# Optimization experiments

Hardware: AMD Instinct MI355X
Metric: run time of the kernel (lower is better)

Reference implementation:

```python
import jax, jax.numpy as jnp
import numpy as np

N = 50000   # nodes
E = 800000  # edges
G = 64      # graphs in batch
H = 64      # hidden_dim
IN = 4      # input_dim (degree-derived features)


def setup_inputs() -> dict:
    key = jax.random.key(0)
    ks = jax.random.split(key, 9)
    src = jax.random.randint(ks[0], (E,), 0, N, dtype=jnp.int32)
    dst = jax.random.randint(ks[1], (E,), 0, N, dtype=jnp.int32)
    graph_ids = jnp.sort(jax.random.randint(ks[2], (N,), 0, G, dtype=jnp.int32))

    def glorot(k, shape):
        fan_in = shape[0]
        return jax.random.normal(k, shape, jnp.float32) / np.float32(np.sqrt(fan_in))

    return dict(
        src=src, dst=dst, graph_ids=graph_ids,
        W1=glorot(ks[3], (IN, H)), b1=jnp.zeros((H,), jnp.float32),
        W2=glorot(ks[4], (H, H)),  b2=jnp.zeros((H,), jnp.float32),
        W3=glorot(ks[5], (H, H)),  b3=jnp.zeros((H,), jnp.float32),
        W4=glorot(ks[6], (H, H)),  b4=jnp.zeros((H,), jnp.float32),
        Wout=glorot(ks[7], (H, 1)), bout=jnp.zeros((1,), jnp.float32),
    )


def _graph_conv(h, src, dst, norm_src, norm_dst, W, b):
    # DGL GraphConv, norm='both': D_dst^{-1/2} * A^T * (D_src^{-1/2} * h) @ W + b
    m = (h * norm_src)[src]                              # [E, F] gather
    agg = jax.ops.segment_sum(m, dst, num_segments=N)    # [N, F] scatter-add
    return (agg * norm_dst) @ W + b


def reference(src, dst, graph_ids, W1, b1, W2, b2, W3, b3, W4, b4, Wout, bout):
    ones_e = jnp.ones((E,), jnp.float32)
    in_deg = jax.ops.segment_sum(ones_e, dst, num_segments=N)   # [N]
    out_deg = jax.ops.segment_sum(ones_e, src, num_segments=N)  # [N]

    # degree-derived node features (exactly as in forward)
    h1 = in_deg[:, None]
    h2 = (in_deg - 3.0 > 0).astype(jnp.float32)[:, None]
    h3 = 3.0 / h1
    h4 = (in_deg - 4.0 > 0).astype(jnp.float32)[:, None]
    h_ = jnp.concatenate([h1, h2, h3, h4], axis=1)               # [N, 4]

    # symmetric norms (DGL clamps degree to >= 1)
    norm_src = jnp.clip(out_deg, 1.0, None)[:, None] ** -0.5     # [N, 1]
    norm_dst = jnp.clip(in_deg, 1.0, None)[:, None] ** -0.5      # [N, 1]

    h = jax.nn.relu(_graph_conv(h_, src, dst, norm_src, norm_dst, W1, b1))
    h = jax.nn.relu(_graph_conv(h, src, dst, norm_src, norm_dst, W2, b2))
    h = jax.nn.relu(_graph_conv(h, src, dst, norm_src, norm_dst, W3, b3))
    h = jax.nn.relu(_graph_conv(h, src, dst, norm_src, norm_dst, W4, b4))

    # dgl.mean_nodes: per-graph mean pooling
    node_counts = jax.ops.segment_sum(jnp.ones((N,), jnp.float32), graph_ids, num_segments=G)
    graph_emb = jax.ops.segment_sum(h, graph_ids, num_segments=G) / node_counts[:, None]

    # dropout = identity at inference
    return jax.nn.sigmoid(graph_emb @ Wout + bout)               # [G, 1]
```

## Files before the change

### kernel.cpp

```cpp
#include <hip/hip_runtime.h>
#include <hip/hip_fp8.h>
#include <math.h>

#define N_NODES 50000
#define N_EDGES 800000
#define NP 4
#define NS 64
#define PSZ (N_NODES / NP)
#define SSZ (N_EDGES / NS)
#define NB 196

typedef _Float16 half8 __attribute__((ext_vector_type(8)));
typedef float floatx4 __attribute__((ext_vector_type(4)));

__device__ __forceinline__ unsigned char f_to_fp8(float f) {
    __hip_fp8_e4m3 q(f);
    return (unsigned char)q.__x;
}
__device__ __forceinline__ float fp8_to_f(unsigned char u) {
    __hip_fp8_e4m3 q;
    q.__x = (__hip_fp8_storage_t)u;
    return (float)q;
}

__global__ __launch_bounds__(256) void hist_wt_kernel(const int* __restrict__ src,
                                                      const int* __restrict__ dst,
                                                      unsigned char* __restrict__ inpart,
                                                      unsigned char* __restrict__ outpart,
                                                      unsigned char* __restrict__ rank,
                                                      const float* __restrict__ W2,
                                                      const float* __restrict__ W3,
                                                      const float* __restrict__ W4,
                                                      _Float16* __restrict__ WT,
                                                      float* __restrict__ gacc) {
    __shared__ int h[PSZ + 4];
    if (blockIdx.x >= NP * NS) {
        int wb = blockIdx.x - NP * NS;
        if (wb < 48) {
            int i = wb * 256 + threadIdx.x;
            if (i < 3 * 4096) {
                int l = i >> 12;
                int r = i & 4095;
                int k = r >> 6, n = r & 63;
                const float* W = (l == 0) ? W2 : (l == 1) ? W3 : W4;
                WT[l * 4096 + n * 64 + k] = (_Float16)W[r];
            }
        } else {
            for (int i = threadIdx.x; i < 64 * 64 + 64; i += 256) gacc[i] = 0.0f;
        }
        return;
    }
    int p = blockIdx.x / NS, s = blockIdx.x % NS;
    for (int i = threadIdx.x; i < (PSZ + 4) / 4; i += 256)
        ((int4*)h)[i] = make_int4(0, 0, 0, 0);
    __syncthreads();
    int lo = p * PSZ;
    int ebase = s * SSZ;
    const int4* d4 = (const int4*)(dst + ebase);
    const int4* s4 = (const int4*)(src + ebase);
    unsigned char* rk = rank + ebase;
    for (int i = threadIdx.x; i < SSZ / 4; i += 256) {
        int4 d = d4[i];
        int4 sv = s4[i];
        int t;
        t = d.x - lo;  if ((unsigned)t < PSZ) rk[4 * i + 0] = (unsigned char)(atomicAdd(&h[t], 1) & 0xffff);
        t = d.y - lo;  if ((unsigned)t < PSZ) rk[4 * i + 1] = (unsigned char)(atomicAdd(&h[t], 1) & 0xffff);
        t = d.z - lo;  if ((unsigned)t < PSZ) rk[4 * i + 2] = (unsigned char)(atomicAdd(&h[t], 1) & 0xffff);
        t = d.w - lo;  if ((unsigned)t < PSZ) rk[4 * i + 3] = (unsigned char)(atomicAdd(&h[t], 1) & 0xffff);
        t = sv.x - lo; if ((unsigned)t < PSZ) atomicAdd(&h[t], 0x10000);
        t = sv.y - lo; if ((unsigned)t < PSZ) atomicAdd(&h[t], 0x10000);
        t = sv.z - lo; if ((unsigned)t < PSZ) atomicAdd(&h[t], 0x10000);
        t = sv.w - lo; if ((unsigned)t < PSZ) atomicAdd(&h[t], 0x10000);
    }
    __syncthreads();
    unsigned char* ip = inpart + (size_t)s * N_NODES + lo;
    unsigned char* op = outpart + (size_t)s * N_NODES + lo;
    for (int i = threadIdx.x; i < PSZ / 2; i += 256) {
        int v0 = h[2 * i], v1 = h[2 * i + 1];
        uchar2 iv, ov;
        iv.x = (unsigned char)(v0 & 0xff);
        iv.y = (unsigned char)(v1 & 0xff);
        ov.x = (unsigned char)((v0 >> 16) & 0xff);
        ov.y = (unsigned char)((v1 >> 16) & 0xff);
        ((uchar2*)ip)[i] = iv;
        ((uchar2*)op)[i] = ov;
    }
}

__global__ void scan_block_feat_kernel(unsigned char* __restrict__ inpart,
                                       const unsigned char* __restrict__ outpart,
                                       const int* __restrict__ graph_ids,
                                       int* __restrict__ row_start, int* __restrict__ blk_sums,
                                       float* __restrict__ norm_src, float* __restrict__ norm_dst,
                                       uchar4* __restrict__ hs0, float* __restrict__ gcnt, int N) {
    __shared__ int ghist[64];
    if (threadIdx.x < 64) ghist[threadIdx.x] = 0;
    int i = blockIdx.x * 256 + threadIdx.x;
    int din_i = 0, dout_i = 0;
    if (i < N) {
        unsigned char run = 0;
#pragma unroll
        for (int s = 0; s < NS; ++s) {
            unsigned char c = inpart[(size_t)s * N_NODES + i];
            inpart[(size_t)s * N_NODES + i] = run;
            run = (unsigned char)(run + c);
            dout_i += outpart[(size_t)s * N_NODES + i];
        }
        din_i = (int)run;
        float din = (float)din_i;
        float dout = (float)dout_i;
        float ns = 1.0f / sqrtf(fmaxf(dout, 1.0f));
        float nd = 1.0f / sqrtf(fmaxf(din, 1.0f));
        norm_src[i] = ns;
        norm_dst[i] = nd;
        float h1 = din;
        float h2 = (din - 3.0f > 0.0f) ? 1.0f : 0.0f;
        float h3 = 3.0f / din;
        float h4 = (din - 4.0f > 0.0f) ? 1.0f : 0.0f;
        uchar4 q;
        q.x = f_to_fp8(h1 * ns);
        q.y = f_to_fp8(h2 * ns);
        q.z = f_to_fp8(h3 * ns);
        q.w = f_to_fp8(h4 * ns);
        hs0[i] = q;
    }
    __syncthreads();
    if (i < N) atomicAdd(&ghist[graph_ids[i]], 1);
    int lane = threadIdx.x & 63;
    int wid = threadIdx.x >> 6;
    int x = din_i;
#pragma unroll
    for (int off = 1; off < 64; off <<= 1) {
        int t = __shfl_up(x, off);
        if (lane >= off) x += t;
    }
    __shared__ int wsum[4];
    if (lane == 63) wsum[wid] = x;
    __syncthreads();
    int woff = 0;
    for (int w = 0; w < wid; ++w) woff += wsum[w];
    int incl = x + woff;
    if (i < N) row_start[i] = incl - din_i;
    if (threadIdx.x == 255) blk_sums[blockIdx.x] = incl;
    if (threadIdx.x < 64 && ghist[threadIdx.x] > 0)
        atomicAdd(&gcnt[threadIdx.x], (float)ghist[threadIdx.x]);
}

__global__ void row_add_kernel(int* __restrict__ row_start,
                               const int* __restrict__ blk_sums, int N) {
    __shared__ int sOff[256];
    int t = threadIdx.x;
    int v = (t < NB) ? blk_sums[t] : 0;
    int lane = t & 63;
    int wid = t >> 6;
    int x = v;
#pragma unroll
    for (int off = 1; off < 64; off <<= 1) {
        int tt = __shfl_up(x, off);
        if (lane >= off) x += tt;
    }
    __shared__ int wsum[4];
    if (lane == 63) wsum[wid] = x;
    __syncthreads();
    int woff = 0;
    for (int w = 0; w < wid; ++w) woff += wsum[w];
    sOff[t] = x + woff - v;
    __syncthreads();
    int i = blockIdx.x * 256 + threadIdx.x;
    if (blockIdx.x == 0 && threadIdx.x == 0) row_start[N] = N_EDGES;
    if (i < N) row_start[i] += sOff[blockIdx.x];
}

__global__ __launch_bounds__(256) void csr_fill_kernel(const int* __restrict__ src,
                                                       const int* __restrict__ dst,
                                                       const int* __restrict__ row_start,
                                                       const unsigned char* __restrict__ inpart,
                                                       const unsigned char* __restrict__ rank,
                                                       unsigned short* __restrict__ csr_src) {
    int i = blockIdx.x * 256 + threadIdx.x;
    if (i >= N_EDGES / 4) return;
    int4 d = ((const int4*)dst)[i];
    int4 sv = ((const int4*)src)[i];
    uchar4 rk = ((const uchar4*)rank)[i];
    int s = (4 * i) / SSZ;
    const unsigned char* pref = inpart + (size_t)s * N_NODES;
    csr_src[row_start[d.x] + (int)pref[d.x] + (int)rk.x] = (unsigned short)sv.x;
    csr_src[row_start[d.y] + (int)pref[d.y] + (int)rk.y] = (unsigned short)sv.y;
    csr_src[row_start[d.z] + (int)pref[d.z] + (int)rk.z] = (unsigned short)sv.z;
    csr_src[row_start[d.w] + (int)pref[d.w] + (int)rk.w] = (unsigned short)sv.w;
}

__global__ void conv4_kernel(const uchar4* __restrict__ hs0,
                             const int* __restrict__ row_start,
                             const unsigned short* __restrict__ csr_src,
                             const float* __restrict__ norm_src,
                             const float* __restrict__ norm_dst,
                             const float* __restrict__ W, const float* __restrict__ b,
                             unsigned char* __restrict__ out, int N) {
    __shared__ float sW[4 * 64];
    __shared__ float sb[64];
    sW[threadIdx.x] = W[threadIdx.x];
    if (threadIdx.x < 64) sb[threadIdx.x] = b[threadIdx.x];
    __syncthreads();
    int lane = threadIdx.x & 63;
    int wid = threadIdx.x >> 6;
    int v = blockIdx.x * 4 + wid;
    if (v >= N) return;
    int rs = row_start[v], re = row_start[v + 1];
    float ax = 0.f, ay = 0.f, az = 0.f, aw = 0.f;
    for (int e = rs + lane; e < re; e += 64) {
        uchar4 f = hs0[csr_src[e]];
        ax += fp8_to_f(f.x); ay += fp8_to_f(f.y);
        az += fp8_to_f(f.z); aw += fp8_to_f(f.w);
    }
#pragma unroll
    for (int off = 32; off; off >>= 1) {
        ax += __shfl_xor(ax, off);
        ay += __shfl_xor(ay, off);
        az += __shfl_xor(az, off);
        aw += __shfl_xor(aw, off);
    }
    float nd = norm_dst[v];
    float r = sb[lane] + nd * (ax * sW[lane] + ay * sW[64 + lane] +
                               az * sW[128 + lane] + aw * sW[192 + lane]);
    r = fmaxf(r, 0.0f) * norm_src[v];
    out[(size_t)v * 64 + lane] = f_to_fp8(r);
}

#define LOADIDX(MY, E0)  MY = (int)csr_src[(E0) + (lane & 15)];

#define GATHER(T, MY)                                                   \
    _Pragma("unroll")                                                   \
    for (int j = 0; j < 16; ++j) {                                      \
        unsigned uu = (unsigned)__builtin_amdgcn_readlane(MY, j);       \
        if (uu >= (unsigned)N_NODES) uu = 0;                            \
        T[j] = hs_in[(uu << 6) + (unsigned)lane];                       \
    }

#define ACCUM(T)                                                        \
    _Pragma("unroll")                                                   \
    for (int j = 0; j < 16; ++j) {                                      \
        while (ecur == bound) {                                         \
            float ndc = __uint_as_float(                                \
                (unsigned)__builtin_amdgcn_readlane((int)nd8u, cur - vbase)); \
            sAgg[wavei][cur - vbase][lane] = (_Float16)(acc * ndc);     \
            acc = 0.0f;                                                 \
            ++cur;                                                      \
            bound = (cur < vend)                                        \
                        ? __builtin_amdgcn_readlane(rb8, cur - vbase)   \
                        : 0x7fffffff;                                   \
        }                                                               \
        acc += fp8_to_f(T[j]);                                         \
        ++ecur;                                                         \
    }

__global__ __launch_bounds__(256) void conv64_kernel(
        const unsigned char* __restrict__ hs_in,
        const int* __restrict__ row_start,
        const unsigned short* __restrict__ csr_src,
        const float* __restrict__ norm_src,
        const float* __restrict__ norm_dst,
        const _Float16* __restrict__ WT, const float* __restrict__ b,
        unsigned char* __restrict__ out8,
        const int* __restrict__ graph_ids, float* __restrict__ gacc,
        int do_pool, int N) {
    __shared__ _Float16 sAgg[4][16][72];
    const int lane = threadIdx.x & 63;
    const int wavei = __builtin_amdgcn_readfirstlane(threadIdx.x >> 6);
    const int vbase = blockIdx.x * 32 + wavei * 8;
    if (vbase >= N) return;

    const int vend = vbase + 8;
    const int rb8 = row_start[vbase + 1 + (lane & 7)];
    const unsigned nd8u = __float_as_uint(norm_dst[vbase + (lane & 7)]);
    const unsigned ns8u = __float_as_uint(norm_src[vbase + (lane & 7)]);
    const int rs = row_start[vbase];
    const int re = __builtin_amdgcn_readlane(rb8, 7);
    int cur = vbase;
    int bound = __builtin_amdgcn_readlane(rb8, 0);
    int ecur = rs;
    float acc = 0.0f;
    int nbp = (re - rs + 15) >> 4;
    int e = rs;
    int myA, myB;
    unsigned char tA[16], tB[16];

    if (nbp > 0) {
        LOADIDX(myA, e);
        GATHER(tA, myA);
        LOADIDX(myB, e + 16);
        int k = 0;
        while (k + 2 <= nbp) {
            GATHER(tB, myB);
            LOADIDX(myA, e + 32);
            ACCUM(tA);
            if (k + 2 < nbp) {
                GATHER(tA, myA);
                LOADIDX(myB, e + 48);
            }
            ACCUM(tB);
            k += 2; e += 32;
        }
        if (k < nbp) { ACCUM(tA); }
    }
    while (cur < vend) {
        float ndc = __uint_as_float(
            (unsigned)__builtin_amdgcn_readlane((int)nd8u, cur - vbase));
        sAgg[wavei][cur - vbase][lane] = (_Float16)(acc * ndc);
        acc = 0.0f;
        ++cur;
    }

    const int l15 = lane & 15;
    const int quad = lane >> 4;
    const _Float16* aRow = &sAgg[wavei][l15][quad * 8];
    half8 a0 = *(const half8*)(aRow);
    half8 a1 = *(const half8*)(aRow + 32);

    floatx4 c[4];
#pragma unroll
    for (int nt = 0; nt < 4; ++nt) c[nt] = (floatx4){0.f, 0.f, 0.f, 0.f};

#pragma unroll
    for (int nt = 0; nt < 4; ++nt) {
        const _Float16* bp = WT + ((size_t)(nt * 16 + l15)) * 64 + quad * 8;
        half8 b0 = *(const half8*)bp;
        half8 b1 = *(const half8*)(bp + 32);
        c[nt] = __builtin_amdgcn_mfma_f32_16x16x32_f16(a0, b0, c[nt], 0, 0, 0);
        c[nt] = __builtin_amdgcn_mfma_f32_16x16x32_f16(a1, b1, c[nt], 0, 0, 0);
    }

    if (do_pool) {
        int g0 = graph_ids[vbase];
        int g7 = graph_ids[vbase + 7];
        if (g0 == g7) {
#pragma unroll
            for (int nt = 0; nt < 4; ++nt) {
                float bias = b[nt * 16 + l15];
                float fsum = 0.0f;
                if (quad < 2) {
#pragma unroll
                    for (int r = 0; r < 4; ++r)
                        fsum += fmaxf(c[nt][r] + bias, 0.0f);
                }
                fsum += __shfl_xor(fsum, 16);
                if (quad == 0)
                    atomicAdd(&gacc[g0 * 64 + nt * 16 + l15], fsum);
            }
        } else {
#pragma unroll
            for (int nt = 0; nt < 4; ++nt) {
                float bias = b[nt * 16 + l15];
#pragma unroll
                for (int r = 0; r < 4; ++r) {
                    int m = quad * 4 + r;
                    if (m < 8) {
                        int v = vbase + m;
                        float val = fmaxf(c[nt][r] + bias, 0.0f);
                        atomicAdd(&gacc[graph_ids[v] * 64 + nt * 16 + l15], val);
                    }
                }
            }
        }
    } else {
#pragma unroll
        for (int nt = 0; nt < 4; ++nt) {
            float bias = b[nt * 16 + l15];
#pragma unroll
            for (int r = 0; r < 4; ++r) {
                int m = quad * 4 + r;
                int v = vbase + m;
                if (m < 8 && v < N) {
                    float nsv = __uint_as_float(
                        (unsigned)__builtin_amdgcn_readlane((int)ns8u, m));
                    float val = fmaxf(c[nt][r] + bias, 0.0f) * nsv;
                    out8[(size_t)v * 64 + nt * 16 + l15] = f_to_fp8(val);
                }
            }
        }
    }
}

__global__ void pool2_kernel(const float* __restrict__ gacc, const float* __restrict__ gcnt,
                             const float* __restrict__ Wout, const float* __restrict__ bout,
                             float* __restrict__ out) {
    int lane = threadIdx.x & 63;
    int g = blockIdx.x * 4 + (threadIdx.x >> 6);
    float p = (gacc[g * 64 + lane] / gcnt[g]) * Wout[lane];
#pragma unroll
    for (int off = 32; off; off >>= 1) p += __shfl_xor(p, off);
    if (lane == 0) out[g] = 1.0f / (1.0f + expf(-(p + bout[0])));
}

extern "C" void kernel_launch(void* const* d_in, const int* in_sizes, int n_in,
                              void* d_out, int out_size, void* d_ws, size_t ws_size,
                              hipStream_t stream) {
    const int* src = (const int*)d_in[0];
    const int* dst = (const int*)d_in[1];
    const int* graph_ids = (const int*)d_in[2];
    const float* W1 = (const float*)d_in[3];
    const float* b1 = (const float*)d_in[4];
    const float* W2 = (const float*)d_in[5];
    const float* b2 = (const float*)d_in[6];
    const float* W3 = (const float*)d_in[7];
    const float* b3 = (const float*)d_in[8];
    const float* W4 = (const float*)d_in[9];
    const float* b4 = (const float*)d_in[10];
    const float* Wout = (const float*)d_in[11];
    const float* bout = (const float*)d_in[12];
    float* out = (float*)d_out;

    const int N = N_NODES, E = N_EDGES;

    unsigned char* buf8A = (unsigned char*)d_ws;
    unsigned char* buf8B = buf8A + (size_t)N * 64;
    _Float16* WT   = (_Float16*)(buf8B + (size_t)N * 64);
    float* gacc = (float*)(WT + 3 * 4096);
    float* gcnt = gacc + 64 * 64;
    unsigned char* hs0 = (unsigned char*)(gcnt + 64);
    float* norm_src = (float*)(hs0 + (size_t)N * 4);
    float* norm_dst = norm_src + N;
    unsigned short* csr_src = (unsigned short*)(norm_dst + N);
    int* row_start = (int*)(csr_src + E);
    int* blk_sums  = row_start + (N + 1);
    unsigned char* inpart  = (unsigned char*)(blk_sums + NB + 1);
    unsigned char* outpart = inpart + (size_t)NS * N;
    unsigned char* rank    = outpart + (size_t)NS * N;

    hist_wt_kernel<<<NP * NS + 49, 256, 0, stream>>>(src, dst, inpart, outpart, rank,
                                                     W2, W3, W4, WT, gacc);
    scan_block_feat_kernel<<<NB, 256, 0, stream>>>(inpart, outpart, graph_ids,
                                                   row_start, blk_sums,
                                                   norm_src, norm_dst, (uchar4*)hs0, gcnt, N);
    row_add_kernel<<<NB, 256, 0, stream>>>(row_start, blk_sums, N);
    csr_fill_kernel<<<(E / 4 + 255) / 256, 256, 0, stream>>>(src, dst, row_start, inpart,
                                                             rank, csr_src);

    conv4_kernel<<<(N + 3) / 4, 256, 0, stream>>>((const uchar4*)hs0, row_start, csr_src,
                                                  norm_src, norm_dst, W1, b1, buf8A, N);
    const int CB = (N + 31) / 32;
    conv64_kernel<<<CB, 256, 0, stream>>>(buf8A, row_start, csr_src, norm_src, norm_dst,
                                          WT + 0 * 4096, b2, buf8B, graph_ids, gacc, 0, N);
    conv64_kernel<<<CB, 256, 0, stream>>>(buf8B, row_start, csr_src, norm_src, norm_dst,
                                          WT + 1 * 4096, b3, buf8A, graph_ids, gacc, 0, N);
    conv64_kernel<<<CB, 256, 0, stream>>>(buf8A, row_start, csr_src, norm_src, norm_dst,
                                          WT + 2 * 4096, b4, (unsigned char*)nullptr,
                                          graph_ids, gacc, 1, N);

    pool2_kernel<<<16, 256, 0, stream>>>(gacc, gcnt, Wout, bout, out);
}
```

Baseline: 211.6 us.

## Use single-wave blocks and triple-buffered gathers in conv64 kernel

Conv64 now launches one 64-thread wave per block covering 8 nodes instead of four waves per block, which shrinks shared memory to one wave's tile and lets the scheduler place waves independently. The edge-gather loop moves from double to triple buffering, so two gather batches are in flight while a third is accumulated, hiding more gather latency. The cost is more registers per thread for the extra buffer, which can lower occupancy, and many more small blocks to launch. The remainder handling after the loop is reworked to drain up to two pending buffers.

```diff
diff --git a/kernel.cpp b/kernel.cpp
--- a/kernel.cpp
+++ b/kernel.cpp
@@ -243,7 +243,7 @@
         while (ecur == bound) {                                         \
             float ndc = __uint_as_float(                                \
                 (unsigned)__builtin_amdgcn_readlane((int)nd8u, cur - vbase)); \
-            sAgg[wavei][cur - vbase][lane] = (_Float16)(acc * ndc);     \
+            sAgg[cur - vbase][lane] = (_Float16)(acc * ndc);            \
             acc = 0.0f;                                                 \
             ++cur;                                                      \
             bound = (cur < vend)                                        \
@@ -254,7 +254,7 @@
         ++ecur;                                                         \
     }
 
-__global__ __launch_bounds__(256) void conv64_kernel(
+__global__ __launch_bounds__(64) void conv64_kernel(
         const unsigned char* __restrict__ hs_in,
         const int* __restrict__ row_start,
         const unsigned short* __restrict__ csr_src,
@@ -264,10 +264,9 @@
         unsigned char* __restrict__ out8,
         const int* __restrict__ graph_ids, float* __restrict__ gacc,
         int do_pool, int N) {
-    __shared__ _Float16 sAgg[4][16][72];
+    __shared__ _Float16 sAgg[16][72];
     const int lane = threadIdx.x & 63;
-    const int wavei = __builtin_amdgcn_readfirstlane(threadIdx.x >> 6);
-    const int vbase = blockIdx.x * 32 + wavei * 8;
+    const int vbase = blockIdx.x * 8;
     if (vbase >= N) return;
 
     const int vend = vbase + 8;
@@ -282,38 +281,37 @@
     float acc = 0.0f;
     int nbp = (re - rs + 15) >> 4;
     int e = rs;
-    int myA, myB;
-    unsigned char tA[16], tB[16];
+    int my0, my1, my2;
+    unsigned char t0[16], t1[16], t2[16];
 
     if (nbp > 0) {
-        LOADIDX(myA, e);
-        GATHER(tA, myA);
-        LOADIDX(myB, e + 16);
+        LOADIDX(my0, e);
+        GATHER(t0, my0);
+        LOADIDX(my1, e + 16);
+        GATHER(t1, my1);
+        LOADIDX(my2, e + 32);
         int k = 0;
-        while (k + 2 <= nbp) {
-            GATHER(tB, myB);
-            LOADIDX(myA, e + 32);
-            ACCUM(tA);
-            if (k + 2 < nbp) {
-                GATHER(tA, myA);
-                LOADIDX(myB, e + 48);
-            }
-            ACCUM(tB);
-            k += 2; e += 32;
+        while (k + 3 <= nbp) {
+            GATHER(t2, my2);  LOADIDX(my0, e + 48);  ACCUM(t0);
+            GATHER(t0, my0);  LOADIDX(my1, e + 64);  ACCUM(t1);
+            GATHER(t1, my1);  LOADIDX(my2, e + 80);  ACCUM(t2);
+            k += 3; e += 48;
         }
-        if (k < nbp) { ACCUM(tA); }
+        int r = nbp - k;
+        if (r >= 1) { ACCUM(t0); }
+        if (r >= 2) { ACCUM(t1); }
     }
     while (cur < vend) {
         float ndc = __uint_as_float(
             (unsigned)__builtin_amdgcn_readlane((int)nd8u, cur - vbase));
-        sAgg[wavei][cur - vbase][lane] = (_Float16)(acc * ndc);
+        sAgg[cur - vbase][lane] = (_Float16)(acc * ndc);
         acc = 0.0f;
         ++cur;
     }
 
     const int l15 = lane & 15;
     const int quad = lane >> 4;
-    const _Float16* aRow = &sAgg[wavei][l15][quad * 8];
+    const _Float16* aRow = &sAgg[l15][quad * 8];
     half8 a0 = *(const half8*)(aRow);
     half8 a1 = *(const half8*)(aRow + 32);
 
@@ -438,14 +436,14 @@
 
     conv4_kernel<<<(N + 3) / 4, 256, 0, stream>>>((const uchar4*)hs0, row_start, csr_src,
                                                   norm_src, norm_dst, W1, b1, buf8A, N);
-    const int CB = (N + 31) / 32;
-    conv64_kernel<<<CB, 256, 0, stream>>>(buf8A, row_start, csr_src, norm_src, norm_dst,
-                                          WT + 0 * 4096, b2, buf8B, graph_ids, gacc, 0, N);
-    conv64_kernel<<<CB, 256, 0, stream>>>(buf8B, row_start, csr_src, norm_src, norm_dst,
-                                          WT + 1 * 4096, b3, buf8A, graph_ids, gacc, 0, N);
-    conv64_kernel<<<CB, 256, 0, stream>>>(buf8A, row_start, csr_src, norm_src, norm_dst,
-                                          WT + 2 * 4096, b4, (unsigned char*)nullptr,
-                                          graph_ids, gacc, 1, N);
+    const int CB = N / 8;
+    conv64_kernel<<<CB, 64, 0, stream>>>(buf8A, row_start, csr_src, norm_src, norm_dst,
+                                         WT + 0 * 4096, b2, buf8B, graph_ids, gacc, 0, N);
+    conv64_kernel<<<CB, 64, 0, stream>>>(buf8B, row_start, csr_src, norm_src, norm_dst,
+                                         WT + 1 * 4096, b3, buf8A, graph_ids, gacc, 0, N);
+    conv64_kernel<<<CB, 64, 0, stream>>>(buf8A, row_start, csr_src, norm_src, norm_dst,
+                                         WT + 2 * 4096, b4, (unsigned char*)nullptr,
+                                         graph_ids, gacc, 1, N);
 
     pool2_kernel<<<16, 256, 0, stream>>>(gacc, gcnt, Wout, bout, out);
 }
```

New measurement: 230.3 us. 1.09x slower.

## Restructure conv64 gather to one node per 16-lane group with 4-byte loads

Applied to the files above, without the earlier changes.

Each wave now handles four nodes, one per 16-lane group, and each lane loads four fp8 features as a 32-bit word. This replaces the serial per-wave walk over 8 nodes, which used per-byte gathers and segment-boundary branching. Blocks now cover 16 nodes that share one block-wide aggregation tile; each wave computes one 16-column slice of the output with two MFMAs after a __syncthreads. Load imbalance between groups in a wave, since lanes run to the maximum degree, and the extra barrier are the tradeoffs.

```diff
diff --git a/kernel.cpp b/kernel.cpp
--- a/kernel.cpp
+++ b/kernel.cpp
@@ -227,33 +227,6 @@
     out[(size_t)v * 64 + lane] = f_to_fp8(r);
 }
 
-#define LOADIDX(MY, E0)  MY = (int)csr_src[(E0) + (lane & 15)];
-
-#define GATHER(T, MY)                                                   \
-    _Pragma("unroll")                                                   \
-    for (int j = 0; j < 16; ++j) {                                      \
-        unsigned uu = (unsigned)__builtin_amdgcn_readlane(MY, j);       \
-        if (uu >= (unsigned)N_NODES) uu = 0;                            \
-        T[j] = hs_in[(uu << 6) + (unsigned)lane];                       \
-    }
-
-#define ACCUM(T)                                                        \
-    _Pragma("unroll")                                                   \
-    for (int j = 0; j < 16; ++j) {                                      \
-        while (ecur == bound) {                                         \
-            float ndc = __uint_as_float(                                \
-                (unsigned)__builtin_amdgcn_readlane((int)nd8u, cur - vbase)); \
-            sAgg[wavei][cur - vbase][lane] = (_Float16)(acc * ndc);     \
-            acc = 0.0f;                                                 \
-            ++cur;                                                      \
-            bound = (cur < vend)                                        \
-                        ? __builtin_amdgcn_readlane(rb8, cur - vbase)   \
-                        : 0x7fffffff;                                   \
-        }                                                               \
-        acc += fp8_to_f(T[j]);                                         \
-        ++ecur;                                                         \
-    }
-
 __global__ __launch_bounds__(256) void conv64_kernel(
         const unsigned char* __restrict__ hs_in,
         const int* __restrict__ row_start,
@@ -264,119 +237,118 @@
         unsigned char* __restrict__ out8,
         const int* __restrict__ graph_ids, float* __restrict__ gacc,
         int do_pool, int N) {
-    __shared__ _Float16 sAgg[4][16][72];
+    __shared__ _Float16 sAgg[16][72];
     const int lane = threadIdx.x & 63;
     const int wavei = __builtin_amdgcn_readfirstlane(threadIdx.x >> 6);
-    const int vbase = blockIdx.x * 32 + wavei * 8;
-    if (vbase >= N) return;
-
-    const int vend = vbase + 8;
-    const int rb8 = row_start[vbase + 1 + (lane & 7)];
-    const unsigned nd8u = __float_as_uint(norm_dst[vbase + (lane & 7)]);
-    const unsigned ns8u = __float_as_uint(norm_src[vbase + (lane & 7)]);
-    const int rs = row_start[vbase];
-    const int re = __builtin_amdgcn_readlane(rb8, 7);
-    int cur = vbase;
-    int bound = __builtin_amdgcn_readlane(rb8, 0);
-    int ecur = rs;
-    float acc = 0.0f;
-    int nbp = (re - rs + 15) >> 4;
-    int e = rs;
-    int myA, myB;
-    unsigned char tA[16], tB[16];
-
-    if (nbp > 0) {
-        LOADIDX(myA, e);
-        GATHER(tA, myA);
-        LOADIDX(myB, e + 16);
-        int k = 0;
-        while (k + 2 <= nbp) {
-            GATHER(tB, myB);
-            LOADIDX(myA, e + 32);
-            ACCUM(tA);
-            if (k + 2 < nbp) {
-                GATHER(tA, myA);
-                LOADIDX(myB, e + 48);
-            }
-            ACCUM(tB);
-            k += 2; e += 32;
-        }
-        if (k < nbp) { ACCUM(tA); }
-    }
-    while (cur < vend) {
-        float ndc = __uint_as_float(
-            (unsigned)__builtin_amdgcn_readlane((int)nd8u, cur - vbase));
-        sAgg[wavei][cur - vbase][lane] = (_Float16)(acc * ndc);
-        acc = 0.0f;
-        ++cur;
-    }
+    const int l16 = lane & 15;
+    const int gsel = (lane >> 4);
+    const int vblock = blockIdx.x * 16;
+    const int node = vblock + wavei * 4 + gsel;
+
+    const int rs = row_start[node];
+    const int deg = row_start[node + 1] - rs;
+
+    int ncg = (deg + 15) >> 4;
+    int m1 = max(ncg, __shfl_xor(ncg, 16));
+    int ncw = max(m1, __shfl_xor(m1, 32));
+
+    float acc0 = 0.f, acc1 = 0.f, acc2 = 0.f, acc3 = 0.f;
+    const int blane = (lane & 48);
+
+    int pos = rs + l16;
+    unsigned pc = (unsigned)pos;
+    if (pc > (unsigned)(N_EDGES - 1)) pc = N_EDGES - 1;
+    int idx = (int)csr_src[pc];
+
+    for (int c = 0; c < ncw; ++c) {
+        int posN = rs + (c + 1) * 16 + l16;
+        unsigned pn = (unsigned)posN;
+        if (pn > (unsigned)(N_EDGES - 1)) pn = N_EDGES - 1;
+        int idxN = (int)csr_src[pn];
+
+        unsigned tv0, tv1, tv2, tv3, tv4, tv5, tv6, tv7;
+        unsigned tv8, tv9, tv10, tv11, tv12, tv13, tv14, tv15;
+#define GLOAD(J, TV)                                                        \
+        {                                                                   \
+            int si = __shfl(idx, blane + (J));                              \
+            TV = *(const unsigned*)(hs_in + (((size_t)(unsigned)si) << 6)   \
+                                    + (l16 << 2));                          \
+        }
+        GLOAD(0, tv0)   GLOAD(1, tv1)   GLOAD(2, tv2)   GLOAD(3, tv3)
+        GLOAD(4, tv4)   GLOAD(5, tv5)   GLOAD(6, tv6)   GLOAD(7, tv7)
+        GLOAD(8, tv8)   GLOAD(9, tv9)   GLOAD(10, tv10) GLOAD(11, tv11)
+        GLOAD(12, tv12) GLOAD(13, tv13) GLOAD(14, tv14) GLOAD(15, tv15)
+#undef GLOAD
+        int cbase = c * 16;
+#define ACC(J, TV)                                                          \
+        {                                                                   \
+            float mk = (cbase + (J) < deg) ? 1.0f : 0.0f;                   \
+            acc0 += mk * fp8_to_f((unsigned char)(TV & 0xff));              \
+            acc1 += mk * fp8_to_f((unsigned char)((TV >> 8) & 0xff));       \
+            acc2 += mk * fp8_to_f((unsigned char)((TV >> 16) & 0xff));      \
+            acc3 += mk * fp8_to_f((unsigned char)((TV >> 24) & 0xff));      \
+        }
+        ACC(0, tv0)   ACC(1, tv1)   ACC(2, tv2)   ACC(3, tv3)
+        ACC(4, tv4)   ACC(5, tv5)   ACC(6, tv6)   ACC(7, tv7)
+        ACC(8, tv8)   ACC(9, tv9)   ACC(10, tv10) ACC(11, tv11)
+        ACC(12, tv12) ACC(13, tv13) ACC(14, tv14) ACC(15, tv15)
+#undef ACC
+        idx = idxN;
+    }
+
+    float nd = norm_dst[node];
+    _Float16 f0 = (_Float16)(acc0 * nd);
+    _Float16 f1 = (_Float16)(acc1 * nd);
+    _Float16 f2 = (_Float16)(acc2 * nd);
+    _Float16 f3 = (_Float16)(acc3 * nd);
+    _Float16* rowp = &sAgg[wavei * 4 + gsel][l16 * 4];
+    rowp[0] = f0; rowp[1] = f1; rowp[2] = f2; rowp[3] = f3;
+    __syncthreads();
 
     const int l15 = lane & 15;
     const int quad = lane >> 4;
-    const _Float16* aRow = &sAgg[wavei][l15][quad * 8];
+    const _Float16* aRow = &sAgg[l15][quad * 8];
     half8 a0 = *(const half8*)(aRow);
     half8 a1 = *(const half8*)(aRow + 32);
 
-    floatx4 c[4];
-#pragma unroll
-    for (int nt = 0; nt < 4; ++nt) c[nt] = (floatx4){0.f, 0.f, 0.f, 0.f};
-
-#pragma unroll
-    for (int nt = 0; nt < 4; ++nt) {
-        const _Float16* bp = WT + ((size_t)(nt * 16 + l15)) * 64 + quad * 8;
-        half8 b0 = *(const half8*)bp;
-        half8 b1 = *(const half8*)(bp + 32);
-        c[nt] = __builtin_amdgcn_mfma_f32_16x16x32_f16(a0, b0, c[nt], 0, 0, 0);
-        c[nt] = __builtin_amdgcn_mfma_f32_16x16x32_f16(a1, b1, c[nt], 0, 0, 0);
-    }
+    const _Float16* bp = WT + ((size_t)(wavei * 16 + l15)) * 64 + quad * 8;
+    half8 b0 = *(const half8*)bp;
+    half8 b1 = *(const half8*)(bp + 32);
+
+    floatx4 cc = (floatx4){0.f, 0.f, 0.f, 0.f};
+    cc = __builtin_amdgcn_mfma_f32_16x16x32_f16(a0, b0, cc, 0, 0, 0);
+    cc = __builtin_amdgcn_mfma_f32_16x16x32_f16(a1, b1, cc, 0, 0, 0);
+
+    const int col = wavei * 16 + l15;
+    float bias = b[col];
 
     if (do_pool) {
-        int g0 = graph_ids[vbase];
-        int g7 = graph_ids[vbase + 7];
-        if (g0 == g7) {
-#pragma unroll
-            for (int nt = 0; nt < 4; ++nt) {
-                float bias = b[nt * 16 + l15];
-                float fsum = 0.0f;
-                if (quad < 2) {
-#pragma unroll
-                    for (int r = 0; r < 4; ++r)
-                        fsum += fmaxf(c[nt][r] + bias, 0.0f);
-                }
-                fsum += __shfl_xor(fsum, 16);
-                if (quad == 0)
-                    atomicAdd(&gacc[g0 * 64 + nt * 16 + l15], fsum);
-            }
+        int g0 = graph_ids[vblock];
+        int g15 = graph_ids[vblock + 15];
+        if (g0 == g15) {
+            float fsum = 0.0f;
+#pragma unroll
+            for (int r = 0; r < 4; ++r)
+                fsum += fmaxf(cc[r] + bias, 0.0f);
+            fsum += __shfl_xor(fsum, 16);
+            fsum += __shfl_xor(fsum, 32);
+            if (quad == 0)
+                atomicAdd(&gacc[g0 * 64 + col], fsum);
         } else {
-#pragma unroll
-            for (int nt = 0; nt < 4; ++nt) {
-                float bias = b[nt * 16 + l15];
-#pragma unroll
-                for (int r = 0; r < 4; ++r) {
-                    int m = quad * 4 + r;
-                    if (m < 8) {
-                        int v = vbase + m;
-                        float val = fmaxf(c[nt][r] + bias, 0.0f);
-                        atomicAdd(&gacc[graph_ids[v] * 64 + nt * 16 + l15], val);
-                    }
-                }
-            }
-        }
-    } else {
-#pragma unroll
-        for (int nt = 0; nt < 4; ++nt) {
-            float bias = b[nt * 16 + l15];
 #pragma unroll
             for (int r = 0; r < 4; ++r) {
                 int m = quad * 4 + r;
-                int v = vbase + m;
-                if (m < 8 && v < N) {
-                    float nsv = __uint_as_float(
-                        (unsigned)__builtin_amdgcn_readlane((int)ns8u, m));
-                    float val = fmaxf(c[nt][r] + bias, 0.0f) * nsv;
-                    out8[(size_t)v * 64 + nt * 16 + l15] = f_to_fp8(val);
-                }
+                float val = fmaxf(cc[r] + bias, 0.0f);
+                atomicAdd(&gacc[graph_ids[vblock + m] * 64 + col], val);
             }
+        }
+    } else {
+#pragma unroll
+        for (int r = 0; r < 4; ++r) {
+            int m = quad * 4 + r;
+            int v = vblock + m;
+            float val = fmaxf(cc[r] + bias, 0.0f) * norm_src[v];
+            out8[(size_t)v * 64 + col] = f_to_fp8(val);
         }
     }
 }
@@ -438,7 +410,7 @@
 
     conv4_kernel<<<(N + 3) / 4, 256, 0, stream>>>((const uchar4*)hs0, row_start, csr_src,
                                                   norm_src, norm_dst, W1, b1, buf8A, N);
-    const int CB = (N + 31) / 32;
+    const int CB = N / 16;
     conv64_kernel<<<CB, 256, 0, stream>>>(buf8A, row_start, csr_src, norm_src, norm_dst,
                                           WT + 0 * 4096, b2, buf8B, graph_ids, gacc, 0, N);
     conv64_kernel<<<CB, 256, 0, stream>>>(buf8B, row_start, csr_src, norm_src, norm_dst,
```

After: 194.0 us. -8.3%, faster.
